# Kernel tuning notes

Hardware: AMD Instinct MI355X
Metric: run time of the kernel (lower is better)

Reference implementation:

```python
import jax, jax.numpy as jnp
import numpy as np

L, D, H, R = 8, 1024, 16, 16
HD = D // H  # head dim


def setup_inputs() -> dict:
    key = jax.random.key(0)
    ks = jax.random.split(key, 7)
    s = 0.02  # init scale for stability
    return {
        "x": jax.random.normal(ks[0], (2, 1024, D), jnp.float32),
        "Wqkv": jax.random.normal(ks[1], (L, D, 3 * D), jnp.float32) * s,
        "Aqkv": jax.random.normal(ks[2], (L, D, R), jnp.float32) * s,
        "Bqkv": jax.random.normal(ks[3], (L, R, 3 * D), jnp.float32) * s,
        "Wproj": jax.random.normal(ks[4], (L, D, D), jnp.float32) * s,
        "Aproj": jax.random.normal(ks[5], (L, D, R), jnp.float32) * s,
        "Bproj": jax.random.normal(ks[6], (L, R, D), jnp.float32) * s,
    }


def _forward(x, Wqkv, Aqkv, Bqkv, Wproj, Aproj, Bproj):
    B, S, _ = x.shape
    # causal mask [S, S]
    mask = jnp.tril(jnp.ones((S, S), bool))

    def layer(h, p):
        Wq, Aq, Bq, Wp, Ap, Bp = p
        # LoRA merge exactly as the module: p + A @ B, then dense matmul
        Wq_m = Wq + Aq @ Bq            # [D, 3D]
        Wp_m = Wp + Ap @ Bp            # [D, D]
        qkv = h @ Wq_m                 # [B, S, 3D]
        q, k, v = jnp.split(qkv, 3, axis=-1)
        q = q.reshape(B, S, H, HD).transpose(0, 2, 1, 3)  # [B,H,S,hd]
        k = k.reshape(B, S, H, HD).transpose(0, 2, 1, 3)
        v = v.reshape(B, S, H, HD).transpose(0, 2, 1, 3)
        scores = jnp.einsum("bhqd,bhkd->bhqk", q, k) / np.sqrt(HD)
        scores = jnp.where(mask, scores, jnp.finfo(scores.dtype).min)
        attn = jax.nn.softmax(scores, axis=-1)
        o = jnp.einsum("bhqk,bhkd->bhqd", attn, v)        # [B,H,S,hd]
        o = o.transpose(0, 2, 1, 3).reshape(B, S, D)
        return h + o @ Wp_m, None

    out, _ = jax.lax.scan(layer, x, (Wqkv, Aqkv, Bqkv, Wproj, Aproj, Bproj))
    return out


def reference(x, Wqkv, Aqkv, Bqkv, Wproj, Aproj, Bproj):
    return _forward(x, Wqkv, Aqkv, Bqkv, Wproj, Aproj, Bproj)
```

## Files before the change

kernel.cpp:

```cpp
#include <hip/hip_runtime.h>
#include <hip/hip_bf16.h>


typedef unsigned short ushort_t;
typedef __attribute__((ext_vector_type(8))) short bf16x8;
typedef __attribute__((ext_vector_type(4))) float f32x4;
typedef __attribute__((ext_vector_type(2))) unsigned int uint32x2;

__device__ __forceinline__ unsigned short f2bf(float f) {
    union { float f; unsigned int u; } x; x.f = f;
    unsigned int r = x.u + 0x7fffu + ((x.u >> 16) & 1u);
    return (unsigned short)(r >> 16);
}

__device__ __forceinline__ unsigned short f2bf_fast(float f) {
    unsigned int r;
    asm("v_cvt_pk_bf16_f32 %0, %1, %2" : "=v"(r) : "v"(f), "v"(0.f));
    return (unsigned short)r;
}

__device__ __forceinline__ unsigned int cvtpk(float lo, float hi) {
    unsigned int r;
    asm("v_cvt_pk_bf16_f32 %0, %1, %2" : "=v"(r) : "v"(lo), "v"(hi));
    return r;
}

__device__ __forceinline__ f32x4 mfma16(bf16x8 a, bf16x8 b, f32x4 c) {
    return __builtin_amdgcn_mfma_f32_16x16x32_bf16(a, b, c, 0, 0, 0);
}

typedef const __attribute__((address_space(1))) unsigned int* gas_ptr;
typedef __attribute__((address_space(3))) unsigned int* las_ptr;
__device__ __forceinline__ void lds_stage16(const void* g, void* l) {
    __builtin_amdgcn_global_load_lds((gas_ptr)(unsigned long long)g,
                                     (las_ptr)(unsigned int)(unsigned long long)l,
                                     16, 0, 0);
}

__global__ __launch_bounds__(256) void convert_x(
    const float4* __restrict__ in, float4* __restrict__ outF,
    ushort4* __restrict__ outB, int n4) {
    int i = blockIdx.x * 256 + threadIdx.x;
    if (i < n4) {
        float4 v = in[i];
        outF[i] = v;
        ushort4 o;
        o.x = f2bf(v.x); o.y = f2bf(v.y); o.z = f2bf(v.z); o.w = f2bf(v.w);
        outB[i] = o;
    }
}

__global__ __launch_bounds__(256) void merge_T2(
    const float* __restrict__ Wq, const float* __restrict__ Aq,
    const float* __restrict__ Bq, unsigned short* __restrict__ WTq,
    const float* __restrict__ Wp, const float* __restrict__ Ap,
    const float* __restrict__ Bp, unsigned short* __restrict__ WTp) {
    __shared__ float Asl[32][17];
    __shared__ __align__(16) float tW[32 * 128];
    int bid = blockIdx.x;
    const float *W, *A, *Bm;
    unsigned short* WT;
    int N, bx, by, bz;
    if (bid < 6144) {
        N = 3072; bx = bid % 24; int u = bid / 24; by = u & 31; bz = u >> 5;
        W = Wq; A = Aq; Bm = Bq; WT = WTq;
    } else {
        bid -= 6144;
        N = 1024; bx = bid & 7; int u = bid >> 3; by = u & 31; bz = u >> 5;
        W = Wp; A = Ap; Bm = Bp; WT = WTp;
    }
    W  += (size_t)bz * 1024 * N;
    A  += (size_t)bz * 1024 * 16;
    Bm += (size_t)bz * 16 * N;
    WT += (size_t)bz * N * 1024;
    const int j0 = bx * 128, i0 = by * 32;
    const int tid = threadIdx.x;
    const int w = tid >> 6, lane = tid & 63;

    #pragma unroll
    for (int s = 0; s < 4; s++) {
        int w4s = w * 4 + s;
        int tr = w4s * 2 + (lane >> 5);
        lds_stage16(W + (size_t)(i0 + tr) * N + j0 + (lane & 31) * 4,
                    (char*)tW + w4s * 1024);
    }
    if (tid < 128) {
        int r = tid >> 2, c4 = (tid & 3) * 4;
        float4 a = *(const float4*)&A[(size_t)(i0 + r) * 16 + c4];
        Asl[r][c4 + 0] = a.x; Asl[r][c4 + 1] = a.y;
        Asl[r][c4 + 2] = a.z; Asl[r][c4 + 3] = a.w;
    }
    const int jj = tid >> 1, half = tid & 1;
    float bcol[16];
    #pragma unroll
    for (int r = 0; r < 16; r++)
        bcol[r] = Bm[(size_t)r * N + j0 + jj];
    __builtin_amdgcn_sched_barrier(0);
    __syncthreads();

    bf16x8 o0, o1;
    #pragma unroll
    for (int c = 0; c < 16; c++) {
        int rloc = half * 16 + c;
        float v = tW[rloc * 128 + jj];
        #pragma unroll
        for (int r = 0; r < 16; r++)
            v += Asl[rloc][r] * bcol[r];
        unsigned short b = f2bf(v);
        if (c < 8) o0[c] = (short)b; else o1[c - 8] = (short)b;
    }
    unsigned short* dst = &WT[(size_t)(j0 + jj) * 1024 + i0 + half * 16];
    *(bf16x8*)dst = o0;
    *(bf16x8*)(dst + 8) = o1;
}

__global__ __launch_bounds__(256) void gemm_qkv(
    const unsigned short* __restrict__ A,
    const unsigned short* __restrict__ BT,
    unsigned short* __restrict__ outB,
    unsigned short* __restrict__ VT,
    int M, int N, int K) {
    __shared__ __align__(16) unsigned short As[2][2][64 * 32];
    __shared__ __align__(16) unsigned short Bs[2][2][128 * 32];
    const int tid = threadIdx.x;
    const int m0 = blockIdx.y * 64, n0 = blockIdx.x * 128;
    const int w = tid >> 6, lane = tid & 63;
    const int wm = (w >> 1) * 32, wn = (w & 1) * 64;
    const int lr = lane & 15, quad = lane >> 4;
    const int srowA = w * 16 + (lane >> 2);
    const int skof = (lane & 3) * 8;

    f32x4 acc[2][4] = {};

    auto stage = [&](int k0, int buf) {
        #pragma unroll
        for (int h = 0; h < 2; h++) {
            lds_stage16(A + (size_t)(m0 + srowA) * K + k0 + h * 32 + skof,
                        (char*)As[buf][h] + w * 1024);
            #pragma unroll
            for (int s = 0; s < 2; s++) {
                int srowB = w * 32 + s * 16 + (lane >> 2);
                lds_stage16(BT + (size_t)(n0 + srowB) * K + k0 + h * 32 + skof,
                            (char*)Bs[buf][h] + (w * 2 + s) * 1024);
            }
        }
    };

    const int nk = K >> 6;
    stage(0, 0);
    for (int t = 0; t < nk; t++) {
        __syncthreads();
        if (t + 1 < nk) stage((t + 1) << 6, (t + 1) & 1);
        const int cur = t & 1;
        #pragma unroll
        for (int h = 0; h < 2; h++) {
            bf16x8 af[2], bfr[4];
            #pragma unroll
            for (int i = 0; i < 2; i++)
                af[i] = *(const bf16x8*)&As[cur][h][(wm + i * 16 + lr) * 32 + quad * 8];
            #pragma unroll
            for (int j = 0; j < 4; j++)
                bfr[j] = *(const bf16x8*)&Bs[cur][h][(wn + j * 16 + lr) * 32 + quad * 8];
            #pragma unroll
            for (int i = 0; i < 2; i++)
                #pragma unroll
                for (int j = 0; j < 4; j++)
                    acc[i][j] = mfma16(af[i], bfr[j], acc[i][j]);
        }
    }
    if (n0 < 2048) {
        #pragma unroll
        for (int i = 0; i < 2; i++)
            #pragma unroll
            for (int j = 0; j < 4; j++)
                #pragma unroll
                for (int r = 0; r < 4; r++) {
                    int row = m0 + wm + i * 16 + quad * 4 + r;
                    int col = n0 + wn + j * 16 + lr;
                    float v = acc[i][j][r];
                    if (col < 1024) v *= 0.125f * 1.44269504f;
                    outB[(size_t)row * N + col] = f2bf(v);
                }
    } else {
        const int b = m0 >> 10;
        #pragma unroll
        for (int i = 0; i < 2; i++) {
            int row0 = m0 + wm + i * 16 + quad * 4;
            int s = row0 & 1023;
            #pragma unroll
            for (int j = 0; j < 4; j++) {
                int hd = n0 - 2048 + wn + j * 16 + lr;
                ushort4 o;
                o.x = f2bf(acc[i][j][0]); o.y = f2bf(acc[i][j][1]);
                o.z = f2bf(acc[i][j][2]); o.w = f2bf(acc[i][j][3]);
                *(ushort4*)&VT[((size_t)b * 1024 + hd) * 1024 + s] = o;
            }
        }
    }
}

__global__ __launch_bounds__(256) void gemm_bf16_64(
    const unsigned short* __restrict__ A,
    const unsigned short* __restrict__ BT,
    const float* __restrict__ res,
    float* __restrict__ outF,
    unsigned short* __restrict__ outB,
    int M, int N, int K) {
    __shared__ __align__(16) unsigned short As[2][2][64 * 32];
    __shared__ __align__(16) unsigned short Bs[2][2][64 * 32];
    const int tid = threadIdx.x;
    const int m0 = blockIdx.y * 64, n0 = blockIdx.x * 64;
    const int w = tid >> 6, lane = tid & 63;
    const int wm = (w >> 1) * 32, wn = (w & 1) * 32;
    const int lr = lane & 15, quad = lane >> 4;
    const int srow = w * 16 + (lane >> 2);
    const int skof = (lane & 3) * 8;

    f32x4 acc[2][2] = {};

    auto stage = [&](int k0, int buf) {
        #pragma unroll
        for (int h = 0; h < 2; h++) {
            lds_stage16(A  + (size_t)(m0 + srow) * K + k0 + h * 32 + skof,
                        (char*)As[buf][h] + w * 1024);
            lds_stage16(BT + (size_t)(n0 + srow) * K + k0 + h * 32 + skof,
                        (char*)Bs[buf][h] + w * 1024);
        }
    };

    const int nk = K >> 6;
    stage(0, 0);
    for (int t = 0; t < nk; t++) {
        __syncthreads();
        if (t + 1 < nk) stage((t + 1) << 6, (t + 1) & 1);
        const int cur = t & 1;
        #pragma unroll
        for (int h = 0; h < 2; h++) {
            bf16x8 af[2], bfr[2];
            #pragma unroll
            for (int i = 0; i < 2; i++) {
                af[i]  = *(const bf16x8*)&As[cur][h][(wm + i * 16 + lr) * 32 + quad * 8];
                bfr[i] = *(const bf16x8*)&Bs[cur][h][(wn + i * 16 + lr) * 32 + quad * 8];
            }
            #pragma unroll
            for (int i = 0; i < 2; i++)
                #pragma unroll
                for (int j = 0; j < 2; j++)
                    acc[i][j] = mfma16(af[i], bfr[j], acc[i][j]);
        }
    }
    #pragma unroll
    for (int i = 0; i < 2; i++)
        #pragma unroll
        for (int j = 0; j < 2; j++)
            #pragma unroll
            for (int r = 0; r < 4; r++) {
                int row = m0 + wm + i * 16 + quad * 4 + r;
                int col = n0 + wn + j * 16 + lr;
                float v = acc[i][j][r] + res[(size_t)row * N + col];
                if (outF) outF[(size_t)row * N + col] = v;
                if (outB) outB[(size_t)row * N + col] = f2bf(v);
            }
}

__global__ __launch_bounds__(256) void attn_kernel(
    const unsigned short* __restrict__ qkv,
    const unsigned short* __restrict__ VT,
    unsigned short* __restrict__ O) {
    __shared__ __align__(16) unsigned short Ks[2][2][128 * 32];
    __shared__ __align__(16) unsigned short Vs[2][4][64 * 32];
    __shared__ __align__(16) unsigned short pls[4][16 * 72];
    const int tid = threadIdx.x;
    const int w = tid >> 6, lane = tid & 63;
    const int lr = lane & 15, quad = lane >> 4;
    const int bh = blockIdx.y, b = bh >> 4, h = bh & 15;
    const int qblk = (bh < 16) ? blockIdx.x : (15 - blockIdx.x);
    const int qb = qblk * 64 + w * 16;
    const int srow = w * 16 + (lane >> 2);
    const int skof = (lane & 3) * 8;

    const size_t rowQ = (size_t)(b * 1024 + qb + lr) * 3072 + h * 64;
    bf16x8 aq0 = *(const bf16x8*)&qkv[rowQ + quad * 8];
    bf16x8 aq1 = *(const bf16x8*)&qkv[rowQ + 32 + quad * 8];

    float m_i = -1e30f, l_i = 0.f;
    f32x4 oacc[4] = {};

    auto stage = [&](int t128, int buf) {
        const int kt = t128 << 7;
        #pragma unroll
        for (int c = 0; c < 2; c++) {
            const size_t gK =
                (size_t)(b * 1024 + kt + c * 64 + srow) * 3072 + 1024 + h * 64;
            lds_stage16(qkv + gK + skof,
                        (char*)Ks[buf][0] + c * 4096 + w * 1024);
            lds_stage16(qkv + gK + 32 + skof,
                        (char*)Ks[buf][1] + c * 4096 + w * 1024);
        }
        const size_t gV = ((size_t)bh * 64 + srow) * 1024 + kt;
        #pragma unroll
        for (int sq = 0; sq < 4; sq++)
            lds_stage16(VT + gV + sq * 32 + skof,
                        (char*)Vs[buf][sq] + w * 1024);
    };

    const int nkt = (qblk + 2) >> 1;
    stage(0, 0);
    for (int t = 0; t < nkt; t++) {
        __syncthreads();
        if (t + 1 < nkt) stage(t + 1, (t + 1) & 1);
        const int cur = t & 1;
        const int kt = t << 7;

        f32x4 s[8] = {};
        #pragma unroll
        for (int nh = 0; nh < 8; nh++) {
            bf16x8 kb0 = *(const bf16x8*)&Ks[cur][0][(nh * 16 + lr) * 32 + quad * 8];
            bf16x8 kb1 = *(const bf16x8*)&Ks[cur][1][(nh * 16 + lr) * 32 + quad * 8];
            s[nh] = mfma16(kb0, aq0, s[nh]);
            s[nh] = mfma16(kb1, aq1, s[nh]);
        }
        if (kt + 128 > qb) {
            const int qrow = qb + lr;
            #pragma unroll
            for (int nh = 0; nh < 8; nh++)
                #pragma unroll
                for (int r = 0; r < 4; r++) {
                    int kcol = kt + nh * 16 + quad * 4 + r;
                    s[nh][r] = (kcol <= qrow) ? s[nh][r] : -1e30f;
                }
        }
        float mx = fmaxf(fmaxf(s[0][0], s[0][1]), fmaxf(s[0][2], s[0][3]));
        #pragma unroll
        for (int nh = 1; nh < 8; nh++)
            mx = fmaxf(mx, fmaxf(fmaxf(s[nh][0], s[nh][1]),
                                 fmaxf(s[nh][2], s[nh][3])));
        mx = fmaxf(mx, __shfl_xor(mx, 16));
        mx = fmaxf(mx, __shfl_xor(mx, 32));
        if (__any(mx > m_i + 8.f)) {
            float mnew = fmaxf(m_i, mx);
            float al = exp2f(m_i - mnew);
            m_i = mnew;
            l_i *= al;
            float alr[4];
            #pragma unroll
            for (int r = 0; r < 4; r++) alr[r] = __shfl(al, quad * 4 + r);
            #pragma unroll
            for (int dt = 0; dt < 4; dt++)
                #pragma unroll
                for (int r = 0; r < 4; r++) oacc[dt][r] *= alr[r];
        }
        float lp = 0.f;
        #pragma unroll
        for (int nh = 0; nh < 8; nh++)
            #pragma unroll
            for (int r = 0; r < 4; r++) {
                float p = exp2f(s[nh][r] - m_i);
                s[nh][r] = p;
                lp += p;
            }
        l_i += lp;
        #pragma unroll
        for (int hp = 0; hp < 2; hp++) {
            #pragma unroll
            for (int n4 = 0; n4 < 4; n4++) {
                int nh = hp * 4 + n4;
                uint32x2 pv;
                pv[0] = cvtpk(s[nh][0], s[nh][1]);
                pv[1] = cvtpk(s[nh][2], s[nh][3]);
                *(uint32x2*)&pls[w][lr * 72 + n4 * 16 + quad * 4] = pv;
            }
            bf16x8 ap0 = *(const bf16x8*)&pls[w][lr * 72 + quad * 8];
            bf16x8 ap1 = *(const bf16x8*)&pls[w][lr * 72 + 32 + quad * 8];
            #pragma unroll
            for (int dt = 0; dt < 4; dt++) {
                bf16x8 vb0 = *(const bf16x8*)
                    &Vs[cur][hp * 2][(dt * 16 + lr) * 32 + quad * 8];
                bf16x8 vb1 = *(const bf16x8*)
                    &Vs[cur][hp * 2 + 1][(dt * 16 + lr) * 32 + quad * 8];
                oacc[dt] = mfma16(ap0, vb0, oacc[dt]);
                oacc[dt] = mfma16(ap1, vb1, oacc[dt]);
            }
        }
    }
    l_i += __shfl_xor(l_i, 16);
    l_i += __shfl_xor(l_i, 32);
    float rl[4];
    #pragma unroll
    for (int r = 0; r < 4; r++) rl[r] = 1.f / __shfl(l_i, quad * 4 + r);
    #pragma unroll
    for (int dt = 0; dt < 4; dt++)
        #pragma unroll
        for (int r = 0; r < 4; r++) {
            int row = b * 1024 + qb + quad * 4 + r;
            int col = h * 64 + dt * 16 + lr;
            O[(size_t)row * 1024 + col] = f2bf_fast(oacc[dt][r] * rl[r]);
        }
}

extern "C" void kernel_launch(void* const* d_in, const int* in_sizes, int n_in,
                              void* d_out, int out_size, void* d_ws, size_t ws_size,
                              hipStream_t stream) {
    const float* x     = (const float*)d_in[0];
    const float* Wqkv  = (const float*)d_in[1];
    const float* Aqkv  = (const float*)d_in[2];
    const float* Bqkv  = (const float*)d_in[3];
    const float* Wproj = (const float*)d_in[4];
    const float* Aproj = (const float*)d_in[5];
    const float* Bproj = (const float*)d_in[6];
    float* out = (float*)d_out;

    char* ws = (char*)d_ws;
    float* h_f32 = (float*)ws;                    ws += (size_t)2048 * 1024 * 4;
    unsigned short* h_bf   = (unsigned short*)ws; ws += (size_t)2048 * 1024 * 2;
    unsigned short* qkv_bf = (unsigned short*)ws; ws += (size_t)2048 * 3072 * 2;
    unsigned short* VT     = (unsigned short*)ws; ws += (size_t)32 * 64 * 1024 * 2;
    unsigned short* O_bf   = (unsigned short*)ws; ws += (size_t)2048 * 1024 * 2;
    unsigned short* WqT8   = (unsigned short*)ws; ws += (size_t)8 * 3072 * 1024 * 2;
    unsigned short* WpT8   = (unsigned short*)ws; ws += (size_t)8 * 1024 * 1024 * 2;

    convert_x<<<2048, 256, 0, stream>>>((const float4*)x, (float4*)h_f32,
                                        (ushort4*)h_bf, 2048 * 1024 / 4);
    merge_T2<<<8192, 256, 0, stream>>>(Wqkv, Aqkv, Bqkv, WqT8,
                                       Wproj, Aproj, Bproj, WpT8);

    for (int l = 0; l < 8; l++) {
        const unsigned short* WqT = WqT8 + (size_t)l * 3072 * 1024;
        const unsigned short* WpT = WpT8 + (size_t)l * 1024 * 1024;
        gemm_qkv<<<dim3(24, 32), 256, 0, stream>>>(h_bf, WqT, qkv_bf, VT,
                                                   2048, 3072, 1024);
        attn_kernel<<<dim3(16, 32), 256, 0, stream>>>(qkv_bf, VT, O_bf);
        float* outF = (l == 7) ? out : h_f32;
        gemm_bf16_64<<<dim3(16, 32), 256, 0, stream>>>(O_bf, WpT, h_f32, outF,
                                                       h_bf, 2048, 1024, 1024);
    }
}
```

Baseline: 653.9 us.

## Replace syncthreads with explicit vmcnt waits and barriers; deepen proj GEMM K-tile

```diff
diff --git a/kernel.cpp b/kernel.cpp
--- a/kernel.cpp
+++ b/kernel.cpp
@@ -35,6 +35,21 @@
     __builtin_amdgcn_global_load_lds((gas_ptr)(unsigned long long)g,
                                      (las_ptr)(unsigned int)(unsigned long long)l,
                                      16, 0, 0);
+}
+
+template <int N>
+__device__ __forceinline__ void wait_vmcnt() {
+    if constexpr (N == 0)      asm volatile("s_waitcnt vmcnt(0)" ::: "memory");
+    else if constexpr (N == 6) asm volatile("s_waitcnt vmcnt(6)" ::: "memory");
+    else                       asm volatile("s_waitcnt vmcnt(8)" ::: "memory");
+}
+__device__ __forceinline__ void hard_barrier() {
+    __builtin_amdgcn_sched_barrier(0);
+    __builtin_amdgcn_s_barrier();
+    __builtin_amdgcn_sched_barrier(0);
+}
+__device__ __forceinline__ void lgkm_drain() {
+    asm volatile("s_waitcnt lgkmcnt(0)" ::: "memory");
 }
 
 __global__ __launch_bounds__(256) void convert_x(
@@ -149,8 +164,9 @@
     const int nk = K >> 6;
     stage(0, 0);
     for (int t = 0; t < nk; t++) {
-        __syncthreads();
-        if (t + 1 < nk) stage((t + 1) << 6, (t + 1) & 1);
+        if (t + 1 < nk) { stage((t + 1) << 6, (t + 1) & 1); wait_vmcnt<6>(); }
+        else wait_vmcnt<0>();
+        hard_barrier();
         const int cur = t & 1;
         #pragma unroll
         for (int h = 0; h < 2; h++) {
@@ -167,6 +183,8 @@
                 for (int j = 0; j < 4; j++)
                     acc[i][j] = mfma16(af[i], bfr[j], acc[i][j]);
         }
+        lgkm_drain();
+        hard_barrier();
     }
     if (n0 < 2048) {
         #pragma unroll
@@ -206,8 +224,8 @@
     float* __restrict__ outF,
     unsigned short* __restrict__ outB,
     int M, int N, int K) {
-    __shared__ __align__(16) unsigned short As[2][2][64 * 32];
-    __shared__ __align__(16) unsigned short Bs[2][2][64 * 32];
+    __shared__ __align__(16) unsigned short As[2][4][64 * 32];
+    __shared__ __align__(16) unsigned short Bs[2][4][64 * 32];
     const int tid = threadIdx.x;
     const int m0 = blockIdx.y * 64, n0 = blockIdx.x * 64;
     const int w = tid >> 6, lane = tid & 63;
@@ -220,7 +238,7 @@
 
     auto stage = [&](int k0, int buf) {
         #pragma unroll
-        for (int h = 0; h < 2; h++) {
+        for (int h = 0; h < 4; h++) {
             lds_stage16(A  + (size_t)(m0 + srow) * K + k0 + h * 32 + skof,
                         (char*)As[buf][h] + w * 1024);
             lds_stage16(BT + (size_t)(n0 + srow) * K + k0 + h * 32 + skof,
@@ -228,14 +246,15 @@
         }
     };
 
-    const int nk = K >> 6;
+    const int nk = K >> 7;
     stage(0, 0);
     for (int t = 0; t < nk; t++) {
-        __syncthreads();
-        if (t + 1 < nk) stage((t + 1) << 6, (t + 1) & 1);
+        if (t + 1 < nk) { stage((t + 1) << 7, (t + 1) & 1); wait_vmcnt<8>(); }
+        else wait_vmcnt<0>();
+        hard_barrier();
         const int cur = t & 1;
         #pragma unroll
-        for (int h = 0; h < 2; h++) {
+        for (int h = 0; h < 4; h++) {
             bf16x8 af[2], bfr[2];
             #pragma unroll
             for (int i = 0; i < 2; i++) {
@@ -248,6 +267,8 @@
                 for (int j = 0; j < 2; j++)
                     acc[i][j] = mfma16(af[i], bfr[j], acc[i][j]);
         }
+        lgkm_drain();
+        hard_barrier();
     }
     #pragma unroll
     for (int i = 0; i < 2; i++)
@@ -307,8 +328,9 @@
     const int nkt = (qblk + 2) >> 1;
     stage(0, 0);
     for (int t = 0; t < nkt; t++) {
-        __syncthreads();
-        if (t + 1 < nkt) stage(t + 1, (t + 1) & 1);
+        if (t + 1 < nkt) { stage(t + 1, (t + 1) & 1); wait_vmcnt<8>(); }
+        else wait_vmcnt<0>();
+        hard_barrier();
         const int cur = t & 1;
         const int kt = t << 7;
 
@@ -382,6 +404,8 @@
                 oacc[dt] = mfma16(ap1, vb1, oacc[dt]);
             }
         }
+        lgkm_drain();
+        hard_barrier();
     }
     l_i += __shfl_xor(l_i, 16);
     l_i += __shfl_xor(l_i, 32);
```

Result: slower. 677.2 us (+3.6%).
